# Kernel tuning notes

Measured on AMD Instinct MI355X. Metric: run time of the kernel, lower is better.

The kernel has to match this reference:

```python
import jax, jax.numpy as jnp
import numpy as np
from jax import lax

T, B, V, N = 128, 256, 256, 1024


def setup_inputs() -> dict:
    key = jax.random.key(0)
    k1, k2, k3, k4 = jax.random.split(key, 4)
    inputs = jax.random.uniform(k1, (T, B, V), dtype=jnp.float32)
    labels = jax.random.uniform(k2, (T * B, V), dtype=jnp.float32)
    weights = jax.random.normal(k3, (V + N, N), dtype=jnp.float32) * 0.1
    bias = jnp.zeros((N,), dtype=jnp.float32)
    output_weights = jax.random.normal(k4, (N, V), dtype=jnp.float32) * 0.1
    output_bias = jnp.zeros((V,), dtype=jnp.float32)
    return {
        "inputs": inputs,
        "labels": labels,
        "weights": weights,
        "bias": bias,
        "output_weights": output_weights,
        "output_bias": output_bias,
    }


def reference(inputs, labels, weights, bias, output_weights, output_bias):
    t, b, v = inputs.shape
    n = weights.shape[1]
    # split concat-matmul into x@Wx + h@Wh (same math as concat([x,h]) @ W)
    w_x = weights[:v]   # [V, N]
    w_h = weights[v:]   # [N, N]

    def step(h, x):
        h_new = jnp.tanh(x @ w_x + h @ w_h + bias)
        return h_new, h_new

    h0 = jnp.zeros((b, n), dtype=inputs.dtype)
    _, outputs = lax.scan(step, h0, inputs)          # [T, B, N]
    outputs = outputs.reshape(t * b, n)              # concat over time
    logits = outputs @ output_weights + output_bias  # [T*B, V]
    # softmax_cross_entropy_with_logits (soft labels), then mean
    log_p = jax.nn.log_softmax(logits, axis=-1)
    loss = jnp.mean(-jnp.sum(labels * log_p, axis=-1))
    return loss
```

## Files before the change

### kernel.cpp

```cpp
#include <hip/hip_runtime.h>
#include <math.h>

typedef __bf16 bf16;
typedef __attribute__((ext_vector_type(4))) __bf16 bf16x4;
typedef __attribute__((ext_vector_type(8))) __bf16 bf16x8;
typedef __attribute__((ext_vector_type(4))) float f32x4;

#define T_STEPS 128
#define B_SZ    256
#define V_SZ    256
#define N_SZ    1024
#define NROWS   (T_STEPS * B_SZ)
#define RSTR    68
#define LSTR    17
#define NGRP    16
#define NCB     16

__device__ __forceinline__ float fast_tanh(float x) {
    float e = __expf(2.0f * x);
    return 1.0f - 2.0f / (e + 1.0f);
}

__global__ void k_convert(const float* __restrict__ src, bf16* __restrict__ dst, int n) {
    int i = (blockIdx.x * blockDim.x + threadIdx.x) * 4;
    if (i < n) {
        float4 v = *(const float4*)(src + i);
        bf16x4 o;
        o.x = (bf16)v.x; o.y = (bf16)v.y; o.z = (bf16)v.z; o.w = (bf16)v.w;
        *(bf16x4*)(dst + i) = o;
    }
}

__global__ void k_transpose_cvt(const float* __restrict__ src, bf16* __restrict__ dst,
                                int R, int C) {
    __shared__ float tile[32][33];
    int c0 = blockIdx.x * 32;
    int r0 = blockIdx.y * 32;
    int tx = threadIdx.x & 31;
    int ty = threadIdx.x >> 5;
#pragma unroll
    for (int i = 0; i < 32; i += 8)
        tile[ty + i][tx] = src[(size_t)(r0 + ty + i) * C + c0 + tx];
    __syncthreads();
#pragma unroll
    for (int i = 0; i < 32; i += 8)
        dst[(size_t)(c0 + ty + i) * R + r0 + tx] = (bf16)tile[tx][ty + i];
}

__global__ __launch_bounds__(512, 2) void k_rnn(
    const bf16* __restrict__ Xb,
    const bf16* __restrict__ Wxt,
    const bf16* __restrict__ Wht,
    const bf16* __restrict__ Wot,
    const float* __restrict__ bias,
    bf16* __restrict__ XH,
    unsigned int* __restrict__ Lgu,
    int* __restrict__ cnt)
{
    __shared__ float red[8 * 16 * RSTR];
    __shared__ float lred[8 * 16 * LSTR];
    const int tid  = threadIdx.x;
    const int lane = tid & 63;
    const int w    = tid >> 6;
    const int quad = lane >> 4;
    const int l15  = lane & 15;
    const int g  = blockIdx.x >> 4;
    const int c  = blockIdx.x & 15;
    const int m0 = g * 16;
    const int n0 = c * 64;
    const int k0 = w * 128;
    const int v0 = w * 32;

    const bf16* Bp = Wht + (size_t)(n0 + l15) * N_SZ + k0 + quad * 8;
    bf16x8 b[4][4];
#pragma unroll
    for (int nt = 0; nt < 4; ++nt)
#pragma unroll
        for (int kc = 0; kc < 4; ++kc)
            b[nt][kc] = *(const bf16x8*)&Bp[(size_t)(nt * 16) * N_SZ + kc * 32];
    bf16x8 bx[4];
#pragma unroll
    for (int nt = 0; nt < 4; ++nt)
        bx[nt] = *(const bf16x8*)&Wxt[(size_t)(n0 + nt * 16 + l15) * V_SZ + v0 + quad * 8];
    bf16x8 bo[4];
#pragma unroll
    for (int kc = 0; kc < 4; ++kc)
        bo[kc] = *(const bf16x8*)&Wot[(size_t)(c * 16 + l15) * N_SZ + k0 + kc * 32 + quad * 8];

    const int orow = tid >> 5;
    const int ocol = (tid & 31) * 2;
    const float bias0 = bias[n0 + ocol];
    const float bias1 = bias[n0 + ocol + 1];
    unsigned int* XHu = (unsigned int*)XH;
    const f32x4 zz = {0.f, 0.f, 0.f, 0.f};

    {
        bf16x8 ax = *(const bf16x8*)&Xb[(size_t)(m0 + l15) * V_SZ + v0 + quad * 8];
        f32x4 acc[4] = {zz, zz, zz, zz};
#pragma unroll
        for (int nt = 0; nt < 4; ++nt)
            acc[nt] = __builtin_amdgcn_mfma_f32_16x16x32_bf16(ax, bx[nt], acc[nt], 0, 0, 0);
#pragma unroll
        for (int nt = 0; nt < 4; ++nt)
#pragma unroll
            for (int r = 0; r < 4; ++r)
                red[(w * 16 + quad * 4 + r) * RSTR + nt * 16 + l15] = acc[nt][r];
        __syncthreads();
        float s0 = bias0, s1 = bias1;
#pragma unroll
        for (int w2 = 0; w2 < 8; ++w2) {
            float2 v = *(const float2*)&red[(w2 * 16 + orow) * RSTR + ocol];
            s0 += v.x; s1 += v.y;
        }
        bf16 r0 = (bf16)fast_tanh(s0);
        bf16 r1 = (bf16)fast_tanh(s1);
        unsigned int outw = (unsigned int)__builtin_bit_cast(unsigned short, r0)
                          | ((unsigned int)__builtin_bit_cast(unsigned short, r1) << 16);
        size_t oidx = (((size_t)0 * B_SZ + m0 + orow) * N_SZ + n0 + ocol) >> 1;
        __hip_atomic_store(&XHu[oidx], outw, __ATOMIC_RELAXED, __HIP_MEMORY_SCOPE_AGENT);
        asm volatile("s_waitcnt vmcnt(0)" ::: "memory");
        __syncthreads();
        if (tid == 0)
            __hip_atomic_fetch_add(&cnt[g * T_STEPS + 0], 1,
                                   __ATOMIC_RELAXED, __HIP_MEMORY_SCOPE_AGENT);
    }

    for (int t = 1; t < T_STEPS; ++t) {
        bf16x8 ax = *(const bf16x8*)&Xb[((size_t)t * B_SZ + m0 + l15) * V_SZ + v0 + quad * 8];

        if (tid == 0) {
            while (__hip_atomic_load(&cnt[g * T_STEPS + t - 1],
                                     __ATOMIC_RELAXED, __HIP_MEMORY_SCOPE_AGENT) < NCB)
                __builtin_amdgcn_s_sleep(2);
        }
        __syncthreads();

        const bf16* Ap = XH + ((size_t)(t - 1) * B_SZ + m0 + l15) * N_SZ + k0 + quad * 8;
        bf16x8 a[4];
#pragma unroll
        for (int kc = 0; kc < 4; ++kc)
            a[kc] = *(const bf16x8*)&Ap[kc * 32];

        f32x4 acc[4] = {zz, zz, zz, zz};
#pragma unroll
        for (int nt = 0; nt < 4; ++nt)
            acc[nt] = __builtin_amdgcn_mfma_f32_16x16x32_bf16(ax, bx[nt], acc[nt], 0, 0, 0);
#pragma unroll
        for (int kc = 0; kc < 4; ++kc)
#pragma unroll
            for (int nt = 0; nt < 4; ++nt)
                acc[nt] = __builtin_amdgcn_mfma_f32_16x16x32_bf16(a[kc], b[nt][kc],
                                                                  acc[nt], 0, 0, 0);

#pragma unroll
        for (int nt = 0; nt < 4; ++nt)
#pragma unroll
            for (int r = 0; r < 4; ++r)
                red[(w * 16 + quad * 4 + r) * RSTR + nt * 16 + l15] = acc[nt][r];
        __syncthreads();

        float s0 = bias0, s1 = bias1;
#pragma unroll
        for (int w2 = 0; w2 < 8; ++w2) {
            float2 v = *(const float2*)&red[(w2 * 16 + orow) * RSTR + ocol];
            s0 += v.x; s1 += v.y;
        }
        bf16 r0 = (bf16)fast_tanh(s0);
        bf16 r1 = (bf16)fast_tanh(s1);
        unsigned int outw = (unsigned int)__builtin_bit_cast(unsigned short, r0)
                          | ((unsigned int)__builtin_bit_cast(unsigned short, r1) << 16);
        size_t oidx = (((size_t)t * B_SZ + m0 + orow) * N_SZ + n0 + ocol) >> 1;
        __hip_atomic_store(&XHu[oidx], outw, __ATOMIC_RELAXED, __HIP_MEMORY_SCOPE_AGENT);
        asm volatile("s_waitcnt vmcnt(0)" ::: "memory");
        __syncthreads();
        if (tid == 0)
            __hip_atomic_fetch_add(&cnt[g * T_STEPS + t], 1,
                                   __ATOMIC_RELAXED, __HIP_MEMORY_SCOPE_AGENT);

        f32x4 lacc = zz;
#pragma unroll
        for (int kc = 0; kc < 4; ++kc)
            lacc = __builtin_amdgcn_mfma_f32_16x16x32_bf16(a[kc], bo[kc], lacc, 0, 0, 0);
#pragma unroll
        for (int r = 0; r < 4; ++r)
            lred[(w * 16 + quad * 4 + r) * LSTR + l15] = lacc[r];
        __syncthreads();
        if (tid < 128) {
            int row = tid >> 3, vp = tid & 7;
            float sa = 0.f, sb = 0.f;
#pragma unroll
            for (int w2 = 0; w2 < 8; ++w2) {
                sa += lred[(w2 * 16 + row) * LSTR + vp * 2];
                sb += lred[(w2 * 16 + row) * LSTR + vp * 2 + 1];
            }
            bf16 pa = (bf16)sa, pb = (bf16)sb;
            unsigned int pw = (unsigned int)__builtin_bit_cast(unsigned short, pa)
                            | ((unsigned int)__builtin_bit_cast(unsigned short, pb) << 16);
            Lgu[(((size_t)(t - 1) * 16 + c) * B_SZ + m0 + row) * 8 + vp] = pw;
        }
        __syncthreads();
    }

    if (tid == 0) {
        while (__hip_atomic_load(&cnt[g * T_STEPS + T_STEPS - 1],
                                 __ATOMIC_RELAXED, __HIP_MEMORY_SCOPE_AGENT) < NCB)
            __builtin_amdgcn_s_sleep(2);
    }
    __syncthreads();
    {
        const bf16* Ap = XH + ((size_t)(T_STEPS - 1) * B_SZ + m0 + l15) * N_SZ + k0 + quad * 8;
        bf16x8 a[4];
#pragma unroll
        for (int kc = 0; kc < 4; ++kc)
            a[kc] = *(const bf16x8*)&Ap[kc * 32];
        f32x4 lacc = zz;
#pragma unroll
        for (int kc = 0; kc < 4; ++kc)
            lacc = __builtin_amdgcn_mfma_f32_16x16x32_bf16(a[kc], bo[kc], lacc, 0, 0, 0);
#pragma unroll
        for (int r = 0; r < 4; ++r)
            lred[(w * 16 + quad * 4 + r) * LSTR + l15] = lacc[r];
        __syncthreads();
        if (tid < 128) {
            int row = tid >> 3, vp = tid & 7;
            float sa = 0.f, sb = 0.f;
#pragma unroll
            for (int w2 = 0; w2 < 8; ++w2) {
                sa += lred[(w2 * 16 + row) * LSTR + vp * 2];
                sb += lred[(w2 * 16 + row) * LSTR + vp * 2 + 1];
            }
            bf16 pa = (bf16)sa, pb = (bf16)sb;
            unsigned int pw = (unsigned int)__builtin_bit_cast(unsigned short, pa)
                            | ((unsigned int)__builtin_bit_cast(unsigned short, pb) << 16);
            Lgu[(((size_t)(T_STEPS - 1) * 16 + c) * B_SZ + m0 + row) * 8 + vp] = pw;
        }
    }
}

__global__ __launch_bounds__(256) void k_lred(
    const bf16* __restrict__ Lg,
    const float* __restrict__ labels,
    const float* __restrict__ ob,
    float* __restrict__ out)
{
    __shared__ float bt[4];
    const int tid  = threadIdx.x;
    const int lane = tid & 63;
    const int w    = tid >> 6;
    const int cs   = lane >> 2;
    const int vi   = (lane & 3) * 4;
    const float4 ob4 = *(const float4*)&ob[cs * 16 + vi];

    float wtot = 0.f;
    for (int i = 0; i < 32; ++i) {
        int row  = blockIdx.x * 128 + w * 32 + i;
        int p    = row >> 8;
        int brow = row & 255;
        bf16x4 lv = *(const bf16x4*)&Lg[(((size_t)p * 16 + cs) * B_SZ + brow) * 16 + vi];
        float l0 = (float)lv.x + ob4.x;
        float l1 = (float)lv.y + ob4.y;
        float l2 = (float)lv.z + ob4.z;
        float l3 = (float)lv.w + ob4.w;
        float mx = fmaxf(fmaxf(l0, l1), fmaxf(l2, l3));
#pragma unroll
        for (int s = 1; s < 64; s <<= 1)
            mx = fmaxf(mx, __shfl_xor(mx, s, 64));
        float sume = __expf(l0 - mx) + __expf(l1 - mx) + __expf(l2 - mx) + __expf(l3 - mx);
        const float4 lb = *(const float4*)&labels[(size_t)row * V_SZ + cs * 16 + vi];
        float labs = lb.x + lb.y + lb.z + lb.w;
        float labv = lb.x * l0 + lb.y * l1 + lb.z * l2 + lb.w * l3;
#pragma unroll
        for (int s = 1; s < 64; s <<= 1) {
            sume += __shfl_xor(sume, s, 64);
            labs += __shfl_xor(labs, s, 64);
            labv += __shfl_xor(labv, s, 64);
        }
        float lse = mx + __logf(sume);
        wtot += labs * lse - labv;
    }
    if (lane == 0) bt[w] = wtot;
    __syncthreads();
    if (tid == 0)
        atomicAdd(out, (bt[0] + bt[1] + bt[2] + bt[3]) * (1.0f / (float)NROWS));
}

extern "C" void kernel_launch(void* const* d_in, const int* in_sizes, int n_in,
                              void* d_out, int out_size, void* d_ws, size_t ws_size,
                              hipStream_t stream)
{
    const float* inputs  = (const float*)d_in[0];
    const float* labels  = (const float*)d_in[1];
    const float* weights = (const float*)d_in[2];
    const float* bias    = (const float*)d_in[3];
    const float* out_w   = (const float*)d_in[4];
    const float* out_b   = (const float*)d_in[5];
    float* out = (float*)d_out;

    char* ws = (char*)d_ws;
    bf16* XH  = (bf16*)ws;  ws += (size_t)NROWS * N_SZ * 2;
    bf16* Xb  = (bf16*)ws;  ws += (size_t)NROWS * V_SZ * 2;
    bf16* Lg  = (bf16*)ws;  ws += (size_t)NROWS * V_SZ * 2;
    bf16* Wxt = (bf16*)ws;  ws += (size_t)N_SZ * V_SZ * 2;
    bf16* Wht = (bf16*)ws;  ws += (size_t)N_SZ * N_SZ * 2;
    bf16* Wot = (bf16*)ws;  ws += (size_t)V_SZ * N_SZ * 2;
    int*  cnt = (int*)ws;   ws += (size_t)NGRP * T_STEPS * 4;

    hipMemsetAsync(out, 0, sizeof(float), stream);
    hipMemsetAsync(cnt, 0, (size_t)NGRP * T_STEPS * 4, stream);

    k_convert<<<dim3(NROWS * V_SZ / 1024), 256, 0, stream>>>(inputs, Xb, NROWS * V_SZ);
    k_transpose_cvt<<<dim3(N_SZ / 32, V_SZ / 32), 256, 0, stream>>>(weights, Wxt, V_SZ, N_SZ);
    k_transpose_cvt<<<dim3(N_SZ / 32, N_SZ / 32), 256, 0, stream>>>(
        weights + (size_t)V_SZ * N_SZ, Wht, N_SZ, N_SZ);
    k_transpose_cvt<<<dim3(V_SZ / 32, N_SZ / 32), 256, 0, stream>>>(out_w, Wot, N_SZ, V_SZ);

    k_rnn<<<dim3(NGRP * NCB), 512, 0, stream>>>(Xb, Wxt, Wht, Wot, bias, XH,
                                                (unsigned int*)Lg, cnt);

    k_lred<<<dim3(NROWS / 128), 256, 0, stream>>>(Lg, labels, out_b, out);
}
```

Baseline: 502.2 us.

## Replace block barriers with per-wave counter signaling in the recurrent step loop

Each wave now signals and waits on the per-group step counter itself, with the counter threshold raised to 16 blocks × 8 waves. This removes the `__syncthreads` around the signal and the wait. The output-logit MFMA is moved up next to the recurrent MFMAs so both partial sums go to shared memory before one barrier, which removes two more barriers per step. The aim is to shorten the serial per-step latency of the 128-step recurrence. In exchange there are more atomic increments and spinning waves, and safe reuse of the shared reduction buffers now depends on the cross-block counter ordering.

```diff
diff --git a/kernel.cpp b/kernel.cpp
--- a/kernel.cpp
+++ b/kernel.cpp
@@ -15,6 +15,7 @@
 #define LSTR    17
 #define NGRP    16
 #define NCB     16
+#define ARRV    (NCB * 8)
 
 __device__ __forceinline__ float fast_tanh(float x) {
     float e = __expf(2.0f * x);
@@ -70,6 +71,7 @@
     const int n0 = c * 64;
     const int k0 = w * 128;
     const int v0 = w * 32;
+    int* gcnt = cnt + g * T_STEPS;
 
     const bf16* Bp = Wht + (size_t)(n0 + l15) * N_SZ + k0 + quad * 8;
     bf16x8 b[4][4];
@@ -91,6 +93,8 @@
     const int ocol = (tid & 31) * 2;
     const float bias0 = bias[n0 + ocol];
     const float bias1 = bias[n0 + ocol + 1];
+    const int lrow = w * 2 + (lane >> 3);
+    const int lvp  = lane & 7;
     unsigned int* XHu = (unsigned int*)XH;
     const f32x4 zz = {0.f, 0.f, 0.f, 0.f};
 
@@ -119,21 +123,18 @@
         size_t oidx = (((size_t)0 * B_SZ + m0 + orow) * N_SZ + n0 + ocol) >> 1;
         __hip_atomic_store(&XHu[oidx], outw, __ATOMIC_RELAXED, __HIP_MEMORY_SCOPE_AGENT);
         asm volatile("s_waitcnt vmcnt(0)" ::: "memory");
-        __syncthreads();
-        if (tid == 0)
-            __hip_atomic_fetch_add(&cnt[g * T_STEPS + 0], 1,
-                                   __ATOMIC_RELAXED, __HIP_MEMORY_SCOPE_AGENT);
+        if (lane == 0)
+            __hip_atomic_fetch_add(&gcnt[0], 1, __ATOMIC_RELAXED, __HIP_MEMORY_SCOPE_AGENT);
     }
 
     for (int t = 1; t < T_STEPS; ++t) {
         bf16x8 ax = *(const bf16x8*)&Xb[((size_t)t * B_SZ + m0 + l15) * V_SZ + v0 + quad * 8];
 
-        if (tid == 0) {
-            while (__hip_atomic_load(&cnt[g * T_STEPS + t - 1],
-                                     __ATOMIC_RELAXED, __HIP_MEMORY_SCOPE_AGENT) < NCB)
-                __builtin_amdgcn_s_sleep(2);
-        }
-        __syncthreads();
+        if (lane == 0) {
+            while (__hip_atomic_load(&gcnt[t - 1], __ATOMIC_RELAXED,
+                                     __HIP_MEMORY_SCOPE_AGENT) < ARRV)
+                __builtin_amdgcn_s_sleep(1);
+        }
 
         const bf16* Ap = XH + ((size_t)(t - 1) * B_SZ + m0 + l15) * N_SZ + k0 + quad * 8;
         bf16x8 a[4];
@@ -151,12 +152,19 @@
             for (int nt = 0; nt < 4; ++nt)
                 acc[nt] = __builtin_amdgcn_mfma_f32_16x16x32_bf16(a[kc], b[nt][kc],
                                                                   acc[nt], 0, 0, 0);
+        f32x4 lacc = zz;
+#pragma unroll
+        for (int kc = 0; kc < 4; ++kc)
+            lacc = __builtin_amdgcn_mfma_f32_16x16x32_bf16(a[kc], bo[kc], lacc, 0, 0, 0);
 
 #pragma unroll
         for (int nt = 0; nt < 4; ++nt)
 #pragma unroll
             for (int r = 0; r < 4; ++r)
                 red[(w * 16 + quad * 4 + r) * RSTR + nt * 16 + l15] = acc[nt][r];
+#pragma unroll
+        for (int r = 0; r < 4; ++r)
+            lred[(w * 16 + quad * 4 + r) * LSTR + l15] = lacc[r];
         __syncthreads();
 
         float s0 = bias0, s1 = bias1;
@@ -171,42 +179,30 @@
                           | ((unsigned int)__builtin_bit_cast(unsigned short, r1) << 16);
         size_t oidx = (((size_t)t * B_SZ + m0 + orow) * N_SZ + n0 + ocol) >> 1;
         __hip_atomic_store(&XHu[oidx], outw, __ATOMIC_RELAXED, __HIP_MEMORY_SCOPE_AGENT);
-        asm volatile("s_waitcnt vmcnt(0)" ::: "memory");
-        __syncthreads();
-        if (tid == 0)
-            __hip_atomic_fetch_add(&cnt[g * T_STEPS + t], 1,
-                                   __ATOMIC_RELAXED, __HIP_MEMORY_SCOPE_AGENT);
-
-        f32x4 lacc = zz;
-#pragma unroll
-        for (int kc = 0; kc < 4; ++kc)
-            lacc = __builtin_amdgcn_mfma_f32_16x16x32_bf16(a[kc], bo[kc], lacc, 0, 0, 0);
-#pragma unroll
-        for (int r = 0; r < 4; ++r)
-            lred[(w * 16 + quad * 4 + r) * LSTR + l15] = lacc[r];
-        __syncthreads();
-        if (tid < 128) {
-            int row = tid >> 3, vp = tid & 7;
+
+        if (lane < 16) {
             float sa = 0.f, sb = 0.f;
 #pragma unroll
             for (int w2 = 0; w2 < 8; ++w2) {
-                sa += lred[(w2 * 16 + row) * LSTR + vp * 2];
-                sb += lred[(w2 * 16 + row) * LSTR + vp * 2 + 1];
+                sa += lred[(w2 * 16 + lrow) * LSTR + lvp * 2];
+                sb += lred[(w2 * 16 + lrow) * LSTR + lvp * 2 + 1];
             }
             bf16 pa = (bf16)sa, pb = (bf16)sb;
             unsigned int pw = (unsigned int)__builtin_bit_cast(unsigned short, pa)
                             | ((unsigned int)__builtin_bit_cast(unsigned short, pb) << 16);
-            Lgu[(((size_t)(t - 1) * 16 + c) * B_SZ + m0 + row) * 8 + vp] = pw;
-        }
-        __syncthreads();
-    }
-
-    if (tid == 0) {
-        while (__hip_atomic_load(&cnt[g * T_STEPS + T_STEPS - 1],
-                                 __ATOMIC_RELAXED, __HIP_MEMORY_SCOPE_AGENT) < NCB)
-            __builtin_amdgcn_s_sleep(2);
-    }
-    __syncthreads();
+            Lgu[(((size_t)(t - 1) * 16 + c) * B_SZ + m0 + lrow) * 8 + lvp] = pw;
+        }
+
+        asm volatile("s_waitcnt vmcnt(0)" ::: "memory");
+        if (lane == 0)
+            __hip_atomic_fetch_add(&gcnt[t], 1, __ATOMIC_RELAXED, __HIP_MEMORY_SCOPE_AGENT);
+    }
+
+    if (lane == 0) {
+        while (__hip_atomic_load(&gcnt[T_STEPS - 1], __ATOMIC_RELAXED,
+                                 __HIP_MEMORY_SCOPE_AGENT) < ARRV)
+            __builtin_amdgcn_s_sleep(1);
+    }
     {
         const bf16* Ap = XH + ((size_t)(T_STEPS - 1) * B_SZ + m0 + l15) * N_SZ + k0 + quad * 8;
         bf16x8 a[4];
@@ -221,18 +217,17 @@
         for (int r = 0; r < 4; ++r)
             lred[(w * 16 + quad * 4 + r) * LSTR + l15] = lacc[r];
         __syncthreads();
-        if (tid < 128) {
-            int row = tid >> 3, vp = tid & 7;
+        if (lane < 16) {
             float sa = 0.f, sb = 0.f;
 #pragma unroll
             for (int w2 = 0; w2 < 8; ++w2) {
-                sa += lred[(w2 * 16 + row) * LSTR + vp * 2];
-                sb += lred[(w2 * 16 + row) * LSTR + vp * 2 + 1];
+                sa += lred[(w2 * 16 + lrow) * LSTR + lvp * 2];
+                sb += lred[(w2 * 16 + lrow) * LSTR + lvp * 2 + 1];
             }
             bf16 pa = (bf16)sa, pb = (bf16)sb;
             unsigned int pw = (unsigned int)__builtin_bit_cast(unsigned short, pa)
                             | ((unsigned int)__builtin_bit_cast(unsigned short, pb) << 16);
-            Lgu[(((size_t)(T_STEPS - 1) * 16 + c) * B_SZ + m0 + row) * 8 + vp] = pw;
+            Lgu[(((size_t)(T_STEPS - 1) * 16 + c) * B_SZ + m0 + lrow) * 8 + lvp] = pw;
         }
     }
 }
```

Result: slower. 794.3 us (+58.2%).
